# Optimization experiments

Hardware: AMD Instinct MI355X
Metric: run time of the kernel (lower is better)

## Reference

```python
import jax, jax.numpy as jnp
import numpy as np

N = 100000   # nodes per branch
E = 1600000  # edges per branch
B = 512      # graphs in batch
D = 256      # input feature dim
C = 27       # number of side-effect labels
NEG_SLOPE = 0.2


def _gat_conv(x, src, dst, W, a_src, a_dst, b):
    """PyG GATConv, heads=1, with self loops. x:[N,din], src/dst:[E+N]."""
    n = x.shape[0]
    h = x @ W                               # [N, dout]
    al_s = h @ a_src                        # [N]
    al_d = h @ a_dst                        # [N]
    e = jax.nn.leaky_relu(al_s[src] + al_d[dst], NEG_SLOPE)  # [E+N]
    # segment softmax over destination nodes (self loops guarantee non-empty)
    m = jax.ops.segment_max(e, dst, num_segments=n)
    w = jnp.exp(e - m[dst])
    denom = jax.ops.segment_sum(w, dst, num_segments=n)
    alpha = w / denom[dst]                  # [E+N]
    out = jax.ops.segment_sum(h[src] * alpha[:, None], dst, num_segments=n)
    return out + b


def _with_self_loops(edge_index, n):
    loop = jnp.arange(n, dtype=edge_index.dtype)
    src = jnp.concatenate([edge_index[0], loop])
    dst = jnp.concatenate([edge_index[1], loop])
    return src, dst


def _mean_pool(x, batch, num_graphs):
    s = jax.ops.segment_sum(x, batch, num_segments=num_graphs)
    cnt = jax.ops.segment_sum(jnp.ones(x.shape[0], x.dtype), batch, num_segments=num_graphs)
    return s / jnp.maximum(cnt, 1.0)[:, None]


def _gat_params(key, din, dout):
    k = jax.random.split(key, 4)
    sc = 1.0 / np.sqrt(din)
    return (jax.random.normal(k[0], (din, dout), jnp.float32) * sc,
            jax.random.normal(k[1], (dout,), jnp.float32) * sc,
            jax.random.normal(k[2], (dout,), jnp.float32) * sc,
            jnp.zeros((dout,), jnp.float32))


def setup_inputs() -> dict:
    key = jax.random.key(0)
    ks = jax.random.split(key, 12)
    inp = {
        'x_s': jax.random.normal(ks[0], (N, D), jnp.float32),
        'x_t': jax.random.normal(ks[1], (N, D), jnp.float32),
        'edge_index_s': jax.random.randint(ks[2], (2, E), 0, N, jnp.int32),
        'edge_index_t': jax.random.randint(ks[3], (2, E), 0, N, jnp.int32),
        'xs_batch': jnp.sort(jax.random.randint(ks[4], (N,), 0, B, jnp.int32)),
        'xt_batch': jnp.sort(jax.random.randint(ks[5], (N,), 0, B, jnp.int32)),
    }
    for name, kk, din, dout in [('s1', ks[6], D, D // 2), ('s2', ks[7], D // 2, D // 4),
                                 ('t1', ks[8], D, D // 2), ('t2', ks[9], D // 2, D // 4)]:
        W, a_s, a_d, b = _gat_params(kk, din, dout)
        inp[f'W_{name}'] = W
        inp[f'a_src_{name}'] = a_s
        inp[f'a_dst_{name}'] = a_d
        inp[f'b_{name}'] = b
    inp['lin_w'] = jax.random.normal(ks[10], (D // 4, C), jnp.float32) / np.sqrt(D // 4)
    inp['lin_b'] = jnp.zeros((C,), jnp.float32)
    return inp


def reference(x_s, x_t,
              W_s1, a_src_s1, a_dst_s1, b_s1,
              W_s2, a_src_s2, a_dst_s2, b_s2,
              W_t1, a_src_t1, a_dst_t1, b_t1,
              W_t2, a_src_t2, a_dst_t2, b_t2,
              lin_w, lin_b,
              edge_index_s, edge_index_t, xs_batch, xt_batch):
    src_s, dst_s = _with_self_loops(edge_index_s, N)
    src_t, dst_t = _with_self_loops(edge_index_t, N)

    x1 = _gat_conv(x_s, src_s, dst_s, W_s1, a_src_s1, a_dst_s1, b_s1)
    x2 = _gat_conv(x1, src_s, dst_s, W_s2, a_src_s2, a_dst_s2, b_s2)
    xs = _mean_pool(x2, xs_batch, B)

    x3 = _gat_conv(x_t, src_t, dst_t, W_t1, a_src_t1, a_dst_t1, b_t1)
    x4 = _gat_conv(x3, src_t, dst_t, W_t2, a_src_t2, a_dst_t2, b_t2)
    xt = _mean_pool(x4, xt_batch, B)

    out = (xs + xt) @ lin_w + lin_b        # [B, C]
    return jax.nn.sigmoid(out)
```

## Files before the change

kernel.cpp:

```cpp
#include <hip/hip_runtime.h>
#include <hip/hip_bf16.h>
#include <math.h>

#define NEG_SLOPE 0.2f

static const int NN = 100000;
static const int EE = 1600000;
static const int BB = 512;
static const int NTOT = 2 * NN;
static const int ETOT = 2 * EE;
static const int NBUK = (NTOT + 511) / 512;
static const int CHUNK = 4096;
static const int NBLK = (ETOT + CHUNK - 1) / CHUNK;
static const int GB = (NN + 63) / 64;

typedef __attribute__((ext_vector_type(8))) short bf16x8;
typedef __attribute__((ext_vector_type(4))) float f32x4;
typedef __attribute__((ext_vector_type(2))) float f32x2;

__device__ __forceinline__ float leaky(float x) { return x >= 0.f ? x : NEG_SLOPE * x; }

__device__ __forceinline__ unsigned short f2b(float f) {
    __hip_bfloat16 h = __float2bfloat16(f);
    return *reinterpret_cast<unsigned short*>(&h);
}
__device__ __forceinline__ float b2f_lo(unsigned v) { return __uint_as_float(v << 16); }
__device__ __forceinline__ float b2f_hi(unsigned v) { return __uint_as_float(v & 0xFFFF0000u); }
__device__ __forceinline__ unsigned packb(float a, float b) {
    return (unsigned)f2b(a) | ((unsigned)f2b(b) << 16);
}
__device__ __forceinline__ void pkfma(f32x2& acc, f32x2 h, f32x2 w) {
    asm("v_pk_fma_f32 %0, %1, %2, %0" : "+v"(acc) : "v"(h), "v"(w));
}
__device__ __forceinline__ f32x2 unpk(unsigned v) {
    f32x2 r;
    r.x = b2f_lo(v);
    r.y = b2f_hi(v);
    return r;
}

__device__ __forceinline__ void gload_lds16(const void* g, void* l) {
    __builtin_amdgcn_global_load_lds(
        (const __attribute__((address_space(1))) void*)g,
        (__attribute__((address_space(3))) void*)l, 16, 0, 0);
}

__global__ void wt_all_kernel(const float* __restrict__ Ws1, const float* __restrict__ Wt1,
                              const float* __restrict__ Ws2, const float* __restrict__ Wt2_,
                              unsigned short* __restrict__ WT1, unsigned short* __restrict__ WT2) {
    int idx = blockIdx.x * blockDim.x + threadIdx.x;
    if (idx < 2 * 256 * 128) {
        int br = idx >= 256 * 128;
        int j = idx - br * 256 * 128;
        int n = j / 256, k = j - n * 256;
        const float* W = br ? Wt1 : Ws1;
        WT1[idx] = f2b(W[(size_t)k * 128 + n]);
    } else {
        int x = idx - 2 * 256 * 128;
        if (x >= 2 * 128 * 64) return;
        int br = x >= 128 * 64;
        int j = x - br * 128 * 64;
        int n = j / 128, k = j - n * 128;
        const float* W = br ? Wt2_ : Ws2;
        WT2[x] = f2b(W[(size_t)k * 64 + n]);
    }
}


__device__ __forceinline__ void bin_body(int b, unsigned char* smem,
                                         const int* __restrict__ src_s, const int* __restrict__ dst_s,
                                         const int* __restrict__ src_t, const int* __restrict__ dst_t,
                                         uint2* __restrict__ region, int* __restrict__ shist) {
    int* hist = (int*)smem;
    int* part = hist + 512;
    int* cur = part + 256;
    uint2* lbuf = (uint2*)(smem + 5120);
    const int t = threadIdx.x;
    const int base = b * CHUNK;
    const int cnt = min(CHUNK, ETOT - base);
    hist[t] = 0; hist[t + 256] = 0;
    __syncthreads();
    unsigned es[16], ed[16];
    #pragma unroll
    for (int i = 0; i < 16; i++) {
        int li = i * 256 + t;
        if (li < cnt) {
            int e = base + li;
            if (e < EE) {
                es[i] = (unsigned)src_s[e];
                ed[i] = (unsigned)dst_s[e];
            } else {
                es[i] = (unsigned)src_t[e - EE] + NN;
                ed[i] = (unsigned)dst_t[e - EE] + NN;
            }
            atomicAdd(&hist[ed[i] >> 9], 1);
        }
    }
    __syncthreads();
    int d0 = hist[2 * t], d1 = hist[2 * t + 1];
    int s = d0 + d1;
    part[t] = s;
    __syncthreads();
    for (int off = 1; off < 256; off <<= 1) {
        int u = (t >= off) ? part[t - off] : 0;
        __syncthreads();
        part[t] += u;
        __syncthreads();
    }
    int ex = part[t] - s;
    cur[2 * t] = ex;
    cur[2 * t + 1] = ex + d0;
    if (2 * t < NBUK + 1) shist[(2 * t) * NBLK + b] = ex;
    if (2 * t + 1 < NBUK + 1) shist[(2 * t + 1) * NBLK + b] = ex + d0;
    __syncthreads();
    #pragma unroll
    for (int i = 0; i < 16; i++) {
        int li = i * 256 + t;
        if (li < cnt) {
            int slot = atomicAdd(&cur[ed[i] >> 9], 1);
            lbuf[slot] = make_uint2(es[i], ed[i]);
        }
    }
    __syncthreads();
    for (int i = t; i < cnt; i += 256) region[base + i] = lbuf[i];
}

__device__ __forceinline__ void gemm1_body(int bid, unsigned char* smem,
                                           const float* __restrict__ Av_s, const float* __restrict__ Av_t,
                                           const unsigned short* __restrict__ WT,
                                           const float* __restrict__ as_s, const float* __restrict__ ad_s,
                                           const float* __restrict__ as_t, const float* __restrict__ ad_t,
                                           unsigned* __restrict__ hb,
                                           float* __restrict__ al_s, float* __restrict__ al_d) {
    constexpr int K = 256, N = 128;
    constexpr int NT2 = 4;
    constexpr int ROWB = 512;
    constexpr int CPR = 32;
    constexpr int IPW = 8;
    constexpr int SWZ = 15;
    constexpr int KBH = 4;

    unsigned char* Atile = smem;
    float* als0 = (float*)(smem + 32768);
    float* ald0 = als0 + 64;

    const int br = (bid >= GB) ? 1 : 0;
    const int lb = bid - br * GB;
    const int t = threadIdx.x;
    const int l = t & 63, w = t >> 6;
    const int wm = w >> 1, wn = w & 1;
    const int rl = l & 15, kh = l >> 4;
    const int row0blk = lb * 64;
    const char* Ab = (const char*)(br ? Av_t : Av_s);
    const unsigned short* WTb = WT + (size_t)br * N * K;
    const float* asv = br ? as_t : as_s;
    const float* adv = br ? ad_t : ad_s;

    f32x4 acc[2][NT2];
    #pragma unroll
    for (int g = 0; g < 2; g++)
        #pragma unroll
        for (int q = 0; q < NT2; q++) acc[g][q] = (f32x4){0.f, 0.f, 0.f, 0.f};

    #pragma unroll
    for (int h = 0; h < 2; h++) {
        #pragma unroll
        for (int i = 0; i < IPW; i++) {
            int c = (i * 4 + w) * 64 + l;
            int row = c / CPR, jp = c % CPR;
            int jg = jp ^ (row & SWZ);
            int rowg = min(row0blk + row, NN - 1);
            const char* src = Ab + ((size_t)rowg * K + h * (K / 2)) * 4 + jg * 16;
            gload_lds16(src, Atile + c * 16);
        }
        bf16x8 Bv[KBH * NT2];
        #pragma unroll
        for (int kb = 0; kb < KBH; kb++)
            #pragma unroll
            for (int q = 0; q < NT2; q++) {
                int c = wn * (N / 2) + q * 16 + rl;
                Bv[kb * NT2 + q] =
                    *(const bf16x8*)(WTb + (size_t)c * K + h * (K / 2) + kb * 32 + kh * 8);
            }
        __syncthreads();
        #pragma unroll
        for (int kb = 0; kb < KBH; kb++) {
            bf16x8 av[2];
            #pragma unroll
            for (int rg = 0; rg < 2; rg++) {
                int r = wm * 32 + rg * 16 + rl;
                int j0 = kb * 8 + kh * 2;
                int j0s = j0 ^ (r & SWZ);
                int j1s = (j0 + 1) ^ (r & SWZ);
                float4 fa = *(const float4*)(Atile + r * ROWB + j0s * 16);
                float4 fb = *(const float4*)(Atile + r * ROWB + j1s * 16);
                union { bf16x8 v; unsigned short u[8]; } au;
                au.u[0] = f2b(fa.x); au.u[1] = f2b(fa.y);
                au.u[2] = f2b(fa.z); au.u[3] = f2b(fa.w);
                au.u[4] = f2b(fb.x); au.u[5] = f2b(fb.y);
                au.u[6] = f2b(fb.z); au.u[7] = f2b(fb.w);
                av[rg] = au.v;
            }
            #pragma unroll
            for (int q = 0; q < NT2; q++) {
                acc[0][q] = __builtin_amdgcn_mfma_f32_16x16x32_bf16(av[0], Bv[kb * NT2 + q], acc[0][q], 0, 0, 0);
                acc[1][q] = __builtin_amdgcn_mfma_f32_16x16x32_bf16(av[1], Bv[kb * NT2 + q], acc[1][q], 0, 0, 0);
            }
        }
        __syncthreads();
    }

    float asr[NT2], adr[NT2];
    #pragma unroll
    for (int q = 0; q < NT2; q++) {
        int c = wn * (N / 2) + q * 16 + rl;
        asr[q] = asv[c];
        adr[q] = adv[c];
    }

    float psA[2][4], pdA[2][4];
    #pragma unroll
    for (int rg = 0; rg < 2; rg++) {
        #pragma unroll
        for (int i = 0; i < 4; i++) {
            float ps = 0.f, pd = 0.f;
            #pragma unroll
            for (int q = 0; q < NT2; q++) {
                float v = acc[rg][q][i];
                ps += v * asr[q];
                pd += v * adr[q];
            }
            #pragma unroll
            for (int off = 1; off < 16; off <<= 1) {
                ps += __shfl_xor(ps, off);
                pd += __shfl_xor(pd, off);
            }
            psA[rg][i] = ps;
            pdA[rg][i] = pd;
        }
    }
    if (wn == 0 && rl == 0) {
        #pragma unroll
        for (int rg = 0; rg < 2; rg++)
            #pragma unroll
            for (int i = 0; i < 4; i++) {
                int rloc = wm * 32 + rg * 16 + kh * 4 + i;
                als0[rloc] = psA[rg][i];
                ald0[rloc] = pdA[rg][i];
            }
    }
    __syncthreads();
    if (wn == 1 && rl == 0) {
        #pragma unroll
        for (int rg = 0; rg < 2; rg++)
            #pragma unroll
            for (int i = 0; i < 4; i++) {
                int rloc = wm * 32 + rg * 16 + kh * 4 + i;
                int rlocal = lb * 64 + rloc;
                if (rlocal < NN) {
                    int g = br * NN + rlocal;
                    al_s[g] = psA[rg][i] + als0[rloc];
                    al_d[g] = pdA[rg][i] + ald0[rloc];
                }
            }
    }
    #pragma unroll
    for (int rg = 0; rg < 2; rg++) {
        #pragma unroll
        for (int i = 0; i < 4; i++) {
            int rlocal = lb * 64 + wm * 32 + rg * 16 + kh * 4 + i;
            bool ok = (rlocal < NN);
            int g = br * NN + rlocal;
            #pragma unroll
            for (int q = 0; q < NT2; q++) {
                float v = acc[rg][q][i];
                float hi = __shfl_xor(v, 1);
                if (ok && !(rl & 1)) {
                    int c = wn * (N / 2) + q * 16 + rl;
                    hb[(size_t)g * (N / 2) + (c >> 1)] = packb(v, hi);
                }
            }
        }
    }
}

__global__ __launch_bounds__(256, 3) void gemm1_bin_kernel(
        const float* __restrict__ Av_s, const float* __restrict__ Av_t,
        const unsigned short* __restrict__ WT,
        const float* __restrict__ as_s, const float* __restrict__ ad_s,
        const float* __restrict__ as_t, const float* __restrict__ ad_t,
        unsigned* __restrict__ hb, float* __restrict__ al_s, float* __restrict__ al_d,
        const int* __restrict__ src_s, const int* __restrict__ dst_s,
        const int* __restrict__ src_t, const int* __restrict__ dst_t,
        uint2* __restrict__ region, int* __restrict__ shist) {
    __shared__ __align__(16) unsigned char smem[38912];
    int bid = blockIdx.x;
    if (bid < NBLK) {
        bin_body(bid, smem, src_s, dst_s, src_t, dst_t, region, shist);
    } else {
        gemm1_body(bid - NBLK, smem, Av_s, Av_t, WT, as_s, ad_s, as_t, ad_t, hb, al_s, al_d);
    }
}

template <int K, int N>
__global__ __launch_bounds__(256, 3) void gemm2_kernel(
        const unsigned short* __restrict__ Ab_s, const unsigned short* __restrict__ Ab_t,
        const unsigned short* __restrict__ WT,
        const float* __restrict__ as_s, const float* __restrict__ ad_s,
        const float* __restrict__ as_t, const float* __restrict__ ad_t,
        unsigned* __restrict__ hb, float* __restrict__ al_s, float* __restrict__ al_d,
        int nblk) {
    constexpr int NT2 = N / 32;
    constexpr int ROWB = (K / 2) * 2;
    constexpr int CPR = ROWB / 16;
    constexpr int STB = 64 * ROWB;
    constexpr int IPW = (STB / 16) / 256;
    constexpr int SWZ = (CPR - 1) < 15 ? (CPR - 1) : 15;
    constexpr int KBH = (K / 2) / 32;

    __shared__ __align__(16) unsigned char Atile[STB];
    __shared__ float als0[64], ald0[64];

    const int bid = blockIdx.x;
    const int br = (bid >= nblk) ? 1 : 0;
    const int lb = bid - br * nblk;
    const int t = threadIdx.x;
    const int l = t & 63, w = t >> 6;
    const int wm = w >> 1, wn = w & 1;
    const int rl = l & 15, kh = l >> 4;
    const int row0blk = lb * 64;
    const char* Ab = (const char*)(br ? Ab_t : Ab_s);
    const unsigned short* WTb = WT + (size_t)br * N * K;
    const float* asv = br ? as_t : as_s;
    const float* adv = br ? ad_t : ad_s;

    f32x4 acc[2][NT2];
    #pragma unroll
    for (int g = 0; g < 2; g++)
        #pragma unroll
        for (int q = 0; q < NT2; q++) acc[g][q] = (f32x4){0.f, 0.f, 0.f, 0.f};

    #pragma unroll
    for (int h = 0; h < 2; h++) {
        #pragma unroll
        for (int i = 0; i < IPW; i++) {
            int c = (i * 4 + w) * 64 + l;
            int row = c / CPR, jp = c % CPR;
            int jg = jp ^ (row & SWZ);
            int rowg = min(row0blk + row, NN - 1);
            const char* src = Ab + ((size_t)rowg * K + h * (K / 2)) * 2 + jg * 16;
            gload_lds16(src, Atile + c * 16);
        }
        bf16x8 Bv[KBH * NT2];
        #pragma unroll
        for (int kb = 0; kb < KBH; kb++)
            #pragma unroll
            for (int q = 0; q < NT2; q++) {
                int c = wn * (N / 2) + q * 16 + rl;
                Bv[kb * NT2 + q] =
                    *(const bf16x8*)(WTb + (size_t)c * K + h * (K / 2) + kb * 32 + kh * 8);
            }
        __syncthreads();
        #pragma unroll
        for (int kb = 0; kb < KBH; kb++) {
            bf16x8 av[2];
            #pragma unroll
            for (int rg = 0; rg < 2; rg++) {
                int r = wm * 32 + rg * 16 + rl;
                int j = kb * 4 + kh;
                int js = j ^ (r & SWZ);
                av[rg] = *(const bf16x8*)(Atile + r * ROWB + js * 16);
            }
            #pragma unroll
            for (int q = 0; q < NT2; q++) {
                acc[0][q] = __builtin_amdgcn_mfma_f32_16x16x32_bf16(av[0], Bv[kb * NT2 + q], acc[0][q], 0, 0, 0);
                acc[1][q] = __builtin_amdgcn_mfma_f32_16x16x32_bf16(av[1], Bv[kb * NT2 + q], acc[1][q], 0, 0, 0);
            }
        }
        __syncthreads();
    }

    float asr[NT2], adr[NT2];
    #pragma unroll
    for (int q = 0; q < NT2; q++) {
        int c = wn * (N / 2) + q * 16 + rl;
        asr[q] = asv[c];
        adr[q] = adv[c];
    }

    float psA[2][4], pdA[2][4];
    #pragma unroll
    for (int rg = 0; rg < 2; rg++) {
        #pragma unroll
        for (int i = 0; i < 4; i++) {
            float ps = 0.f, pd = 0.f;
            #pragma unroll
            for (int q = 0; q < NT2; q++) {
                float v = acc[rg][q][i];
                ps += v * asr[q];
                pd += v * adr[q];
            }
            #pragma unroll
            for (int off = 1; off < 16; off <<= 1) {
                ps += __shfl_xor(ps, off);
                pd += __shfl_xor(pd, off);
            }
            psA[rg][i] = ps;
            pdA[rg][i] = pd;
        }
    }
    if (wn == 0 && rl == 0) {
        #pragma unroll
        for (int rg = 0; rg < 2; rg++)
            #pragma unroll
            for (int i = 0; i < 4; i++) {
                int rloc = wm * 32 + rg * 16 + kh * 4 + i;
                als0[rloc] = psA[rg][i];
                ald0[rloc] = pdA[rg][i];
            }
    }
    __syncthreads();
    if (wn == 1 && rl == 0) {
        #pragma unroll
        for (int rg = 0; rg < 2; rg++)
            #pragma unroll
            for (int i = 0; i < 4; i++) {
                int rloc = wm * 32 + rg * 16 + kh * 4 + i;
                int rlocal = lb * 64 + rloc;
                if (rlocal < NN) {
                    int g = br * NN + rlocal;
                    al_s[g] = psA[rg][i] + als0[rloc];
                    al_d[g] = pdA[rg][i] + ald0[rloc];
                }
            }
    }
    #pragma unroll
    for (int rg = 0; rg < 2; rg++) {
        #pragma unroll
        for (int i = 0; i < 4; i++) {
            int rlocal = lb * 64 + wm * 32 + rg * 16 + kh * 4 + i;
            bool ok = (rlocal < NN);
            int g = br * NN + rlocal;
            #pragma unroll
            for (int q = 0; q < NT2; q++) {
                float v = acc[rg][q][i];
                float hi = __shfl_xor(v, 1);
                if (ok && !(rl & 1)) {
                    int c = wn * (N / 2) + q * 16 + rl;
                    hb[(size_t)g * (N / 2) + (c >> 1)] = packb(v, hi);
                }
            }
        }
    }
}

__global__ void bucket_tot_kernel(const int* __restrict__ shist, int* __restrict__ btot) {
    __shared__ int red[256];
    const int k = blockIdx.x, t = threadIdx.x;
    int s = 0;
    for (int b = t; b < NBLK; b += 256)
        s += shist[(k + 1) * NBLK + b] - shist[k * NBLK + b];
    red[t] = s;
    __syncthreads();
    for (int off = 128; off > 0; off >>= 1) {
        if (t < off) red[t] += red[t + off];
        __syncthreads();
    }
    if (t == 0) btot[k] = red[0];
}

__global__ void bucket_scan_kernel(const int* __restrict__ btot, int* __restrict__ bbase) {
    __shared__ int part[256];
    int t = threadIdx.x;
    int v0 = (2 * t < NBUK) ? btot[2 * t] : 0;
    int v1 = (2 * t + 1 < NBUK) ? btot[2 * t + 1] : 0;
    int s = v0 + v1;
    part[t] = s;
    __syncthreads();
    for (int off = 1; off < 256; off <<= 1) {
        int u = (t >= off) ? part[t - off] : 0;
        __syncthreads();
        part[t] += u;
        __syncthreads();
    }
    int ex = part[t] - s;
    if (2 * t < NBUK) bbase[2 * t] = ex;
    if (2 * t + 1 < NBUK) bbase[2 * t + 1] = ex + v0;
}

__global__ __launch_bounds__(256) void csr_bucket_kernel(const uint2* __restrict__ region,
                                                         const int* __restrict__ shist,
                                                         const int* __restrict__ bbase,
                                                         int* __restrict__ rowptr,
                                                         int* __restrict__ col) {
    __shared__ int deg[512];
    __shared__ int part[256];
    __shared__ int cur[512];
    const int k = blockIdx.x, t = threadIdx.x;
    const int n0 = k * 512;
    const int nloc = min(512, NTOT - n0);
    const int base = bbase[k];
    deg[t] = 0; deg[t + 256] = 0;
    __syncthreads();
    for (int b = t; b < NBLK; b += 256) {
        int s0 = shist[k * NBLK + b], s1 = shist[(k + 1) * NBLK + b];
        for (int i = s0; i < s1; i++) {
            uint2 e = region[(size_t)b * CHUNK + i];
            atomicAdd(&deg[(int)e.y - n0], 1);
        }
    }
    __syncthreads();
    int d0 = deg[2 * t], d1 = deg[2 * t + 1];
    int s = d0 + d1;
    part[t] = s;
    __syncthreads();
    for (int off = 1; off < 256; off <<= 1) {
        int u = (t >= off) ? part[t - off] : 0;
        __syncthreads();
        part[t] += u;
        __syncthreads();
    }
    int ex = part[t] - s;
    cur[2 * t] = ex;
    cur[2 * t + 1] = ex + d0;
    if (2 * t < nloc) rowptr[n0 + 2 * t] = base + ex;
    if (2 * t + 1 < nloc) rowptr[n0 + 2 * t + 1] = base + ex + d0;
    if (t == 0 && n0 + nloc == NTOT) rowptr[NTOT] = base + part[255];
    __syncthreads();
    for (int b = t; b < NBLK; b += 256) {
        int s0 = shist[k * NBLK + b], s1 = shist[(k + 1) * NBLK + b];
        for (int i = s0; i < s1; i++) {
            uint2 e = region[(size_t)b * CHUNK + i];
            int pos = atomicAdd(&cur[(int)e.y - n0], 1);
            col[base + pos] = (int)e.x;
        }
    }
}

__global__ void gat_gather128_kernel(const int* __restrict__ rowptr, const int* __restrict__ col,
                                     const float* __restrict__ al_s, const float* __restrict__ al_d,
                                     const unsigned* __restrict__ hb,
                                     const float* __restrict__ bias_s,
                                     const float* __restrict__ bias_t,
                                     unsigned* __restrict__ outb) {
    int node = blockIdx.x * 4 + (threadIdx.x >> 6);
    int lane = threadIdx.x & 63;
    if (node >= NTOT) return;
    const float* bias = (node < NN) ? bias_s : bias_t;
    const int slot = lane >> 4, sub = lane & 15;
    const int beg = rowptr[node], end = rowptr[node + 1];
    const float ald = al_d[node];
    const float e_self = leaky(al_s[node] + ald);

    f32x2 acc2[4];
    #pragma unroll
    for (int k = 0; k < 4; k++) acc2[k] = (f32x2){0.f, 0.f};
    float dsum = 0.f;
    for (int base = beg; base < end; base += 64) {
        int i = base + lane;
        float w = 0.f; int s = 0;
        if (i < end) {
            s = col[i];
            w = expf(leaky(al_s[s] + ald));
        }
        dsum += w;
        int cnt = min(64, end - base);
        for (int j = 0; j < cnt; j += 8) {
            int idx0 = j + slot, idx1 = j + 4 + slot;
            float w0 = __shfl(w, idx0), w1 = __shfl(w, idx1);
            int s0 = __shfl(s, idx0), s1 = __shfl(s, idx1);
            uint4 v0 = *(const uint4*)(hb + (size_t)s0 * 64 + sub * 4);
            uint4 v1 = *(const uint4*)(hb + (size_t)s1 * 64 + sub * 4);
            f32x2 wp0 = (f32x2){w0, w0}, wp1 = (f32x2){w1, w1};
            pkfma(acc2[0], unpk(v0.x), wp0);
            pkfma(acc2[1], unpk(v0.y), wp0);
            pkfma(acc2[2], unpk(v0.z), wp0);
            pkfma(acc2[3], unpk(v0.w), wp0);
            pkfma(acc2[0], unpk(v1.x), wp1);
            pkfma(acc2[1], unpk(v1.y), wp1);
            pkfma(acc2[2], unpk(v1.z), wp1);
            pkfma(acc2[3], unpk(v1.w), wp1);
        }
    }
    float acc[8];
    #pragma unroll
    for (int k = 0; k < 4; k++) { acc[2 * k] = acc2[k].x; acc[2 * k + 1] = acc2[k].y; }
    #pragma unroll
    for (int k = 0; k < 8; k++) {
        acc[k] += __shfl_xor(acc[k], 16);
        acc[k] += __shfl_xor(acc[k], 32);
    }
    #pragma unroll
    for (int off = 32; off > 0; off >>= 1) dsum += __shfl_xor(dsum, off);

    float wself = expf(e_self);
    dsum += wself;
    float inv = 1.f / dsum;
    if (slot == 0) {
        uint4 sv = *(const uint4*)(hb + (size_t)node * 64 + sub * 4);
        float sf[8] = { b2f_lo(sv.x), b2f_hi(sv.x), b2f_lo(sv.y), b2f_hi(sv.y),
                        b2f_lo(sv.z), b2f_hi(sv.z), b2f_lo(sv.w), b2f_hi(sv.w) };
        float o[8];
        #pragma unroll
        for (int k = 0; k < 8; k++)
            o[k] = bias[sub * 8 + k] + (acc[k] + wself * sf[k]) * inv;
        uint4 r = make_uint4(packb(o[0], o[1]), packb(o[2], o[3]),
                             packb(o[4], o[5]), packb(o[6], o[7]));
        *(uint4*)(outb + (size_t)node * 64 + sub * 4) = r;
    }
}

__global__ void gat_gather64_kernel(const int* __restrict__ rowptr, const int* __restrict__ col,
                                    const float* __restrict__ al_s, const float* __restrict__ al_d,
                                    const unsigned* __restrict__ hb,
                                    const float* __restrict__ bias_s,
                                    const float* __restrict__ bias_t,
                                    float* __restrict__ out) {
    int node = blockIdx.x * 4 + (threadIdx.x >> 6);
    int lane = threadIdx.x & 63;
    if (node >= NTOT) return;
    const float* bias = (node < NN) ? bias_s : bias_t;
    const int slot = lane >> 4, sub = lane & 15;
    const int beg = rowptr[node], end = rowptr[node + 1];
    const float ald = al_d[node];
    const float e_self = leaky(al_s[node] + ald);

    f32x2 acc2[2];
    acc2[0] = (f32x2){0.f, 0.f};
    acc2[1] = (f32x2){0.f, 0.f};
    float dsum = 0.f;
    for (int base = beg; base < end; base += 64) {
        int i = base + lane;
        float w = 0.f; int s = 0;
        if (i < end) {
            s = col[i];
            w = expf(leaky(al_s[s] + ald));
        }
        dsum += w;
        int cnt = min(64, end - base);
        for (int j = 0; j < cnt; j += 8) {
            int idx0 = j + slot, idx1 = j + 4 + slot;
            float w0 = __shfl(w, idx0), w1 = __shfl(w, idx1);
            int s0 = __shfl(s, idx0), s1 = __shfl(s, idx1);
            uint2 v0 = *(const uint2*)(hb + (size_t)s0 * 32 + sub * 2);
            uint2 v1 = *(const uint2*)(hb + (size_t)s1 * 32 + sub * 2);
            f32x2 wp0 = (f32x2){w0, w0}, wp1 = (f32x2){w1, w1};
            pkfma(acc2[0], unpk(v0.x), wp0);
            pkfma(acc2[1], unpk(v0.y), wp0);
            pkfma(acc2[0], unpk(v1.x), wp1);
            pkfma(acc2[1], unpk(v1.y), wp1);
        }
    }
    float acc[4] = { acc2[0].x, acc2[0].y, acc2[1].x, acc2[1].y };
    #pragma unroll
    for (int k = 0; k < 4; k++) {
        acc[k] += __shfl_xor(acc[k], 16);
        acc[k] += __shfl_xor(acc[k], 32);
    }
    #pragma unroll
    for (int off = 32; off > 0; off >>= 1) dsum += __shfl_xor(dsum, off);

    float wself = expf(e_self);
    dsum += wself;
    float inv = 1.f / dsum;
    if (slot == 0) {
        uint2 sv = *(const uint2*)(hb + (size_t)node * 32 + sub * 2);
        float sf[4] = { b2f_lo(sv.x), b2f_hi(sv.x), b2f_lo(sv.y), b2f_hi(sv.y) };
        float4 o;
        o.x = bias[sub * 4 + 0] + (acc[0] + wself * sf[0]) * inv;
        o.y = bias[sub * 4 + 1] + (acc[1] + wself * sf[1]) * inv;
        o.z = bias[sub * 4 + 2] + (acc[2] + wself * sf[2]) * inv;
        o.w = bias[sub * 4 + 3] + (acc[3] + wself * sf[3]) * inv;
        *(float4*)(out + (size_t)node * 64 + sub * 4) = o;
    }
}

__global__ void pool_seg_kernel(const float* __restrict__ x,
                                const int* __restrict__ bs, const int* __restrict__ bt,
                                float* __restrict__ pooled_s, float* __restrict__ pooled_t) {
    __shared__ float red[4][64];
    __shared__ int bnd[2];
    int g = blockIdx.x;
    int tb = g >= BB;
    int gb = g - tb * BB;
    const int* batch = tb ? bt : bs;
    float* pooled = tb ? pooled_t : pooled_s;
    int off = tb ? NN : 0;
    if (threadIdx.x < 2) {
        int target = gb + threadIdx.x;
        int lo = 0, hi = NN;
        while (lo < hi) {
            int mid = (lo + hi) >> 1;
            if (batch[mid] < target) lo = mid + 1; else hi = mid;
        }
        bnd[threadIdx.x] = lo;
    }
    __syncthreads();
    int beg = bnd[0], end = bnd[1];
    int lane = threadIdx.x & 63, w = threadIdx.x >> 6;
    float acc = 0.f;
    for (int n = beg + w; n < end; n += 4)
        acc += x[(size_t)(off + n) * 64 + lane];
    red[w][lane] = acc;
    __syncthreads();
    if (w == 0) {
        float s = red[0][lane] + red[1][lane] + red[2][lane] + red[3][lane];
        float cnt = (float)(end - beg);
        pooled[(size_t)gb * 64 + lane] = s / fmaxf(cnt, 1.f);
    }
}

__global__ void final_kernel(const float* __restrict__ ps, const float* __restrict__ pt,
                             const float* __restrict__ lw, const float* __restrict__ lb,
                             float* __restrict__ out) {
    int g = blockIdx.x;
    int c = threadIdx.x;
    if (c >= 27) return;
    float acc = lb[c];
    #pragma unroll 8
    for (int k = 0; k < 64; k++) {
        float xv = ps[g * 64 + k] + pt[g * 64 + k];
        acc += xv * lw[k * 27 + c];
    }
    out[g * 27 + c] = 1.f / (1.f + expf(-acc));
}

extern "C" void kernel_launch(void* const* d_in, const int* in_sizes, int n_in,
                              void* d_out, int out_size, void* d_ws, size_t ws_size,
                              hipStream_t stream) {
    const float* x_s = (const float*)d_in[0];
    const float* x_t = (const float*)d_in[1];
    const int* ei_s = (const int*)d_in[2];
    const int* ei_t = (const int*)d_in[3];
    const int* xs_batch = (const int*)d_in[4];
    const int* xt_batch = (const int*)d_in[5];
    const float* W_s1 = (const float*)d_in[6];
    const float* a_src_s1 = (const float*)d_in[7];
    const float* a_dst_s1 = (const float*)d_in[8];
    const float* b_s1 = (const float*)d_in[9];
    const float* W_s2 = (const float*)d_in[10];
    const float* a_src_s2 = (const float*)d_in[11];
    const float* a_dst_s2 = (const float*)d_in[12];
    const float* b_s2 = (const float*)d_in[13];
    const float* W_t1 = (const float*)d_in[14];
    const float* a_src_t1 = (const float*)d_in[15];
    const float* a_dst_t1 = (const float*)d_in[16];
    const float* b_t1 = (const float*)d_in[17];
    const float* W_t2 = (const float*)d_in[18];
    const float* a_src_t2 = (const float*)d_in[19];
    const float* a_dst_t2 = (const float*)d_in[20];
    const float* b_t2 = (const float*)d_in[21];
    const float* lin_w = (const float*)d_in[22];
    const float* lin_b = (const float*)d_in[23];
    float* out = (float*)d_out;

    unsigned* hb = (unsigned*)d_ws;
    unsigned* out1b = hb + (size_t)NTOT * 64;
    float* out2 = (float*)out1b;
    uint2* region = (uint2*)(out1b + (size_t)NTOT * 64);
    int* col = (int*)(region + (size_t)NBLK * CHUNK);
    float* al_s = (float*)(col + ETOT);
    float* al_d = al_s + NTOT;
    float* pooled_s = al_d + NTOT;
    float* pooled_t = pooled_s + (size_t)BB * 64;
    unsigned short* WT1 = (unsigned short*)(pooled_t + (size_t)BB * 64);
    unsigned short* WT2 = WT1 + 2 * 256 * 128;
    int* rowptr = (int*)(WT2 + 2 * 128 * 64);
    int* shist = rowptr + NTOT + 1;
    int* btot = shist + (NBUK + 1) * NBLK;
    int* bbase = btot + NBUK;

    const int* src_s = ei_s;
    const int* dst_s = ei_s + EE;
    const int* src_t = ei_t;
    const int* dst_t = ei_t + EE;

    wt_all_kernel<<<(2 * 256 * 128 + 2 * 128 * 64 + 255) / 256, 256, 0, stream>>>(
        W_s1, W_t1, W_s2, W_t2, WT1, WT2);

    gemm1_bin_kernel<<<NBLK + 2 * GB, 256, 0, stream>>>(
        x_s, x_t, WT1, a_src_s1, a_dst_s1, a_src_t1, a_dst_t1, hb, al_s, al_d,
        src_s, dst_s, src_t, dst_t, region, shist);

    bucket_tot_kernel<<<NBUK, 256, 0, stream>>>(shist, btot);
    bucket_scan_kernel<<<1, 256, 0, stream>>>(btot, bbase);
    csr_bucket_kernel<<<NBUK, 256, 0, stream>>>(region, shist, bbase, rowptr, col);

    gat_gather128_kernel<<<(NTOT + 3) / 4, 256, 0, stream>>>(
        rowptr, col, al_s, al_d, hb, b_s1, b_t1, out1b);

    gemm2_kernel<128, 64><<<2 * GB, 256, 0, stream>>>(
        (const unsigned short*)out1b, (const unsigned short*)out1b + (size_t)NN * 128, WT2,
        a_src_s2, a_dst_s2, a_src_t2, a_dst_t2, hb, al_s, al_d, GB);
    gat_gather64_kernel<<<(NTOT + 3) / 4, 256, 0, stream>>>(
        rowptr, col, al_s, al_d, hb, b_s2, b_t2, out2);

    pool_seg_kernel<<<2 * BB, 256, 0, stream>>>(out2, xs_batch, xt_batch, pooled_s, pooled_t);
    final_kernel<<<BB, 32, 0, stream>>>(pooled_s, pooled_t, lin_w, lin_b, out);
}
```

Before: 451.3 us.

## Fuse mean pooling into second GAT gather via atomics and inline bucket scan

Folds the bucket prefix scan into the CSR build kernel: each block reduces the bucket totals that precede it, so the separate scan launch goes away. The second-layer gather now accumulates its outputs directly into per-graph pooled sums with atomicAdd, which removes the full node-feature write and the separate pooling kernel. The final kernel finds the graph boundaries by binary search and applies the mean normalization. The trade-off is heavy atomic contention on 512×64 pooled addresses, since nodes are sorted by graph, plus a nondeterministic summation order.

```diff
diff --git a/kernel.cpp b/kernel.cpp
--- a/kernel.cpp
+++ b/kernel.cpp
@@ -66,7 +66,6 @@
     }
 }
 
-
 __device__ __forceinline__ void bin_body(int b, unsigned char* smem,
                                          const int* __restrict__ src_s, const int* __restrict__ dst_s,
                                          const int* __restrict__ src_t, const int* __restrict__ dst_t,
@@ -469,28 +468,9 @@
     if (t == 0) btot[k] = red[0];
 }
 
-__global__ void bucket_scan_kernel(const int* __restrict__ btot, int* __restrict__ bbase) {
-    __shared__ int part[256];
-    int t = threadIdx.x;
-    int v0 = (2 * t < NBUK) ? btot[2 * t] : 0;
-    int v1 = (2 * t + 1 < NBUK) ? btot[2 * t + 1] : 0;
-    int s = v0 + v1;
-    part[t] = s;
-    __syncthreads();
-    for (int off = 1; off < 256; off <<= 1) {
-        int u = (t >= off) ? part[t - off] : 0;
-        __syncthreads();
-        part[t] += u;
-        __syncthreads();
-    }
-    int ex = part[t] - s;
-    if (2 * t < NBUK) bbase[2 * t] = ex;
-    if (2 * t + 1 < NBUK) bbase[2 * t + 1] = ex + v0;
-}
-
 __global__ __launch_bounds__(256) void csr_bucket_kernel(const uint2* __restrict__ region,
                                                          const int* __restrict__ shist,
-                                                         const int* __restrict__ bbase,
+                                                         const int* __restrict__ btot,
                                                          int* __restrict__ rowptr,
                                                          int* __restrict__ col) {
     __shared__ int deg[512];
@@ -499,8 +479,17 @@
     const int k = blockIdx.x, t = threadIdx.x;
     const int n0 = k * 512;
     const int nloc = min(512, NTOT - n0);
-    const int base = bbase[k];
+    int bacc = 0;
+    for (int i = t; i < NBUK; i += 256)
+        if (i < k) bacc += btot[i];
+    part[t] = bacc;
     deg[t] = 0; deg[t + 256] = 0;
+    __syncthreads();
+    for (int off = 128; off > 0; off >>= 1) {
+        if (t < off) part[t] += part[t + off];
+        __syncthreads();
+    }
+    const int base = part[0];
     __syncthreads();
     for (int b = t; b < NBLK; b += 256) {
         int s0 = shist[k * NBLK + b], s1 = shist[(k + 1) * NBLK + b];
@@ -615,7 +604,8 @@
                                     const unsigned* __restrict__ hb,
                                     const float* __restrict__ bias_s,
                                     const float* __restrict__ bias_t,
-                                    float* __restrict__ out) {
+                                    const int* __restrict__ bs, const int* __restrict__ bt,
+                                    float* __restrict__ pooled_s, float* __restrict__ pooled_t) {
     int node = blockIdx.x * 4 + (threadIdx.x >> 6);
     int lane = threadIdx.x & 63;
     if (node >= NTOT) return;
@@ -666,63 +656,46 @@
     if (slot == 0) {
         uint2 sv = *(const uint2*)(hb + (size_t)node * 32 + sub * 2);
         float sf[4] = { b2f_lo(sv.x), b2f_hi(sv.x), b2f_lo(sv.y), b2f_hi(sv.y) };
-        float4 o;
-        o.x = bias[sub * 4 + 0] + (acc[0] + wself * sf[0]) * inv;
-        o.y = bias[sub * 4 + 1] + (acc[1] + wself * sf[1]) * inv;
-        o.z = bias[sub * 4 + 2] + (acc[2] + wself * sf[2]) * inv;
-        o.w = bias[sub * 4 + 3] + (acc[3] + wself * sf[3]) * inv;
-        *(float4*)(out + (size_t)node * 64 + sub * 4) = o;
-    }
-}
-
-__global__ void pool_seg_kernel(const float* __restrict__ x,
-                                const int* __restrict__ bs, const int* __restrict__ bt,
-                                float* __restrict__ pooled_s, float* __restrict__ pooled_t) {
-    __shared__ float red[4][64];
-    __shared__ int bnd[2];
+        int nid = (node < NN) ? node : node - NN;
+        const int* batch = (node < NN) ? bs : bt;
+        float* pooled = (node < NN) ? pooled_s : pooled_t;
+        int g = batch[nid];
+        float* pp = pooled + (size_t)g * 64 + sub * 4;
+        atomicAdd(pp + 0, bias[sub * 4 + 0] + (acc[0] + wself * sf[0]) * inv);
+        atomicAdd(pp + 1, bias[sub * 4 + 1] + (acc[1] + wself * sf[1]) * inv);
+        atomicAdd(pp + 2, bias[sub * 4 + 2] + (acc[2] + wself * sf[2]) * inv);
+        atomicAdd(pp + 3, bias[sub * 4 + 3] + (acc[3] + wself * sf[3]) * inv);
+    }
+}
+
+__global__ void final_kernel(const float* __restrict__ ps, const float* __restrict__ pt,
+                             const int* __restrict__ bs, const int* __restrict__ bt,
+                             const float* __restrict__ lw, const float* __restrict__ lb,
+                             float* __restrict__ out) {
+    __shared__ int bnd[4];
     int g = blockIdx.x;
-    int tb = g >= BB;
-    int gb = g - tb * BB;
-    const int* batch = tb ? bt : bs;
-    float* pooled = tb ? pooled_t : pooled_s;
-    int off = tb ? NN : 0;
-    if (threadIdx.x < 2) {
-        int target = gb + threadIdx.x;
+    int tid = threadIdx.x;
+    if (tid < 4) {
+        const int* batch = (tid < 2) ? bs : bt;
+        int target = g + (tid & 1);
         int lo = 0, hi = NN;
         while (lo < hi) {
             int mid = (lo + hi) >> 1;
             if (batch[mid] < target) lo = mid + 1; else hi = mid;
         }
-        bnd[threadIdx.x] = lo;
-    }
-    __syncthreads();
-    int beg = bnd[0], end = bnd[1];
-    int lane = threadIdx.x & 63, w = threadIdx.x >> 6;
-    float acc = 0.f;
-    for (int n = beg + w; n < end; n += 4)
-        acc += x[(size_t)(off + n) * 64 + lane];
-    red[w][lane] = acc;
-    __syncthreads();
-    if (w == 0) {
-        float s = red[0][lane] + red[1][lane] + red[2][lane] + red[3][lane];
-        float cnt = (float)(end - beg);
-        pooled[(size_t)gb * 64 + lane] = s / fmaxf(cnt, 1.f);
-    }
-}
-
-__global__ void final_kernel(const float* __restrict__ ps, const float* __restrict__ pt,
-                             const float* __restrict__ lw, const float* __restrict__ lb,
-                             float* __restrict__ out) {
-    int g = blockIdx.x;
-    int c = threadIdx.x;
-    if (c >= 27) return;
-    float acc = lb[c];
+        bnd[tid] = lo;
+    }
+    __syncthreads();
+    if (tid >= 27) return;
+    float ics = 1.f / fmaxf((float)(bnd[1] - bnd[0]), 1.f);
+    float ict = 1.f / fmaxf((float)(bnd[3] - bnd[2]), 1.f);
+    float acc = lb[tid];
     #pragma unroll 8
     for (int k = 0; k < 64; k++) {
-        float xv = ps[g * 64 + k] + pt[g * 64 + k];
-        acc += xv * lw[k * 27 + c];
-    }
-    out[g * 27 + c] = 1.f / (1.f + expf(-acc));
+        float xv = ps[g * 64 + k] * ics + pt[g * 64 + k] * ict;
+        acc += xv * lw[k * 27 + tid];
+    }
+    out[g * 27 + tid] = 1.f / (1.f + expf(-acc));
 }
 
 extern "C" void kernel_launch(void* const* d_in, const int* in_sizes, int n_in,
@@ -756,7 +729,6 @@
 
     unsigned* hb = (unsigned*)d_ws;
     unsigned* out1b = hb + (size_t)NTOT * 64;
-    float* out2 = (float*)out1b;
     uint2* region = (uint2*)(out1b + (size_t)NTOT * 64);
     int* col = (int*)(region + (size_t)NBLK * CHUNK);
     float* al_s = (float*)(col + ETOT);
@@ -768,13 +740,14 @@
     int* rowptr = (int*)(WT2 + 2 * 128 * 64);
     int* shist = rowptr + NTOT + 1;
     int* btot = shist + (NBUK + 1) * NBLK;
-    int* bbase = btot + NBUK;
 
     const int* src_s = ei_s;
     const int* dst_s = ei_s + EE;
     const int* src_t = ei_t;
     const int* dst_t = ei_t + EE;
 
+    hipMemsetAsync(pooled_s, 0, (size_t)BB * 64 * 2 * sizeof(float), stream);
+
     wt_all_kernel<<<(2 * 256 * 128 + 2 * 128 * 64 + 255) / 256, 256, 0, stream>>>(
         W_s1, W_t1, W_s2, W_t2, WT1, WT2);
 
@@ -783,8 +756,7 @@
         src_s, dst_s, src_t, dst_t, region, shist);
 
     bucket_tot_kernel<<<NBUK, 256, 0, stream>>>(shist, btot);
-    bucket_scan_kernel<<<1, 256, 0, stream>>>(btot, bbase);
-    csr_bucket_kernel<<<NBUK, 256, 0, stream>>>(region, shist, bbase, rowptr, col);
+    csr_bucket_kernel<<<NBUK, 256, 0, stream>>>(region, shist, btot, rowptr, col);
 
     gat_gather128_kernel<<<(NTOT + 3) / 4, 256, 0, stream>>>(
         rowptr, col, al_s, al_d, hb, b_s1, b_t1, out1b);
@@ -793,8 +765,7 @@
         (const unsigned short*)out1b, (const unsigned short*)out1b + (size_t)NN * 128, WT2,
         a_src_s2, a_dst_s2, a_src_t2, a_dst_t2, hb, al_s, al_d, GB);
     gat_gather64_kernel<<<(NTOT + 3) / 4, 256, 0, stream>>>(
-        rowptr, col, al_s, al_d, hb, b_s2, b_t2, out2);
-
-    pool_seg_kernel<<<2 * BB, 256, 0, stream>>>(out2, xs_batch, xt_batch, pooled_s, pooled_t);
-    final_kernel<<<BB, 32, 0, stream>>>(pooled_s, pooled_t, lin_w, lin_b, out);
-}
+        rowptr, col, al_s, al_d, hb, b_s2, b_t2, xs_batch, xt_batch, pooled_s, pooled_t);
+
+    final_kernel<<<BB, 32, 0, stream>>>(pooled_s, pooled_t, xs_batch, xt_batch, lin_w, lin_b, out);
+}
```

New measurement: 668.4 us. 1.48x slower.
